# Optimization experiments

Hardware: AMD Instinct MI355X
Metric: run time of the kernel (lower is better)

The kernel has to match this reference:

```python
import jax, jax.numpy as jnp
import numpy as np

B, S, D, H = 2, 2048, 768, 12
DK = D // H


def setup_inputs() -> dict:
    key = jax.random.key(0)
    ks = jax.random.split(key, 10)
    sc = 0.02
    return {
        "k": jax.random.normal(ks[0], (B, S, D), jnp.float32),
        "q": jax.random.normal(ks[1], (B, S, D), jnp.float32),
        "v": jax.random.normal(ks[2], (B, S, D), jnp.float32),
        "mask": jnp.ones((B, 1, S, S), jnp.int32),
        "wq": jax.random.normal(ks[3], (D, D), jnp.float32) * sc,
        "bq": jnp.zeros((D,), jnp.float32),
        "wk": jax.random.normal(ks[4], (D, D), jnp.float32) * sc,
        "bk": jnp.zeros((D,), jnp.float32),
        "wv": jax.random.normal(ks[5], (D, D), jnp.float32) * sc,
        "bv": jnp.zeros((D,), jnp.float32),
        "wo": jax.random.normal(ks[6], (D, D), jnp.float32) * sc,
        "bo": jnp.zeros((D,), jnp.float32),
    }


def reference(k, q, v, mask, wq, bq, wk, bk, wv, bv, wo, bo):
    # Linear projections (torch Linear: x @ W^T + b)
    query = q @ wq.T + bq
    key_ = k @ wk.T + bk
    value = v @ wv.T + bv
    # [B,S,D] -> [B,H,S,DK]
    def split_heads(x):
        return x.reshape(B, S, H, DK).transpose(0, 2, 1, 3)
    Q, K, V = split_heads(query), split_heads(key_), split_heads(value)
    # NOTE: original masked_fill result is discarded -> mask is a no-op.
    scores = jnp.einsum("bhqd,bhkd->bhqk", Q, K) / jnp.sqrt(jnp.float32(DK))
    attn = jax.nn.softmax(scores, axis=-1)  # dropout p=0.0 -> identity
    out = jnp.einsum("bhqk,bhkd->bhqd", attn, V)
    out = out.transpose(0, 2, 1, 3).reshape(B, S, D)
    return out @ wo.T + bo
```

## Files before the change

### kernel.cpp

```cpp
#include <hip/hip_runtime.h>
#include <hip/hip_bf16.h>

#define B_  2
#define S_  2048
#define D_  768
#define H_  12
#define DK_ 64
#define NX_ (B_*S_*D_)
#define NW_ (D_*D_)
#define NR_ (B_*H_*S_)

typedef __attribute__((ext_vector_type(8))) short  bf16x8;
typedef __attribute__((ext_vector_type(4))) float  f32x4;

__device__ __forceinline__ unsigned short f2bf(float f) {
    unsigned int u = __float_as_uint(f);
    u += 0x7fffu + ((u >> 16) & 1u);
    return (unsigned short)(u >> 16);
}

__device__ __forceinline__ void async_cp16(const unsigned short* g,
                                           const unsigned short* lds_uniform_base) {
    __builtin_amdgcn_global_load_lds(
        (const __attribute__((address_space(1))) unsigned int*)(uintptr_t)g,
        (__attribute__((address_space(3))) unsigned int*)(unsigned int)(uintptr_t)lds_uniform_base,
        16, 0, 0);
}

__global__ __launch_bounds__(256) void cvt_w(const float* __restrict__ w0,
                                             const float* __restrict__ w1,
                                             const float* __restrict__ w2,
                                             const float* __restrict__ w3,
                                             unsigned short* __restrict__ dst) {
    const float* src[4] = {w0, w1, w2, w3};
    const int widx = blockIdx.y;
    const int idx  = blockIdx.x * 256 + threadIdx.x;
    const int n = idx / 96;
    const int g = idx % 96;
    const float4 f0 = *(const float4*)(src[widx] + (long)n * D_ + g * 8);
    const float4 f1 = *(const float4*)(src[widx] + (long)n * D_ + g * 8 + 4);
    unsigned short o[8] = {f2bf(f0.x), f2bf(f0.y), f2bf(f0.z), f2bf(f0.w),
                           f2bf(f1.x), f2bf(f1.y), f2bf(f1.z), f2bf(f1.w)};
    const int kdst = (g >> 3) * 64 + (((g & 7) ^ (n & 7)) * 8);
    *(uint4*)(dst + (long)widx * NW_ + (long)n * D_ + kdst) = *(const uint4*)o;
}

struct QkvArgs {
    const float* X[3];
    const float* bias[3];
    unsigned short* out[3];
};

__global__ __launch_bounds__(256, 2) void gemm_qkv(QkvArgs args,
                                                   const unsigned short* __restrict__ Wsw) {
    __shared__ __align__(16) unsigned short smem[17408];
    unsigned short* As = smem;
    unsigned short* Bs = smem + 8192;

    const int t    = threadIdx.x;
    const int wave = t >> 6;
    const int lane = t & 63;
    const int l16  = lane & 15;
    const int quad = lane >> 4;
    const int wm   = wave >> 1, wn = wave & 1;
    const int m0   = blockIdx.x * 128;
    const int zz   = blockIdx.y / 6;
    const int nb   = blockIdx.y % 6;
    const int n0   = nb * 128;

    const float* Xp = args.X[zz];
    const unsigned short* Wp = Wsw + (long)zz * NW_;

    f32x4 acc[4][4];
#pragma unroll
    for (int s = 0; s < 4; s++)
#pragma unroll
        for (int j = 0; j < 4; j++) acc[s][j] = (f32x4){0.f, 0.f, 0.f, 0.f};

    const int arow = t >> 3;
    const int acg  = t & 7;
    const int brow = lane >> 3;
    const int bcg  = lane & 7;

    for (int k0 = 0; k0 < D_; k0 += 64) {
        __syncthreads();
#pragma unroll
        for (int i = 0; i < 4; i++) {
            const int chunk = wave * 4 + i;
            async_cp16(Wp + (long)(n0 + chunk * 8 + brow) * D_ + k0 + bcg * 8,
                       Bs + chunk * 512);
        }
#pragma unroll
        for (int p = 0; p < 4; p++) {
            const int r = p * 32 + arow;
            const float4 f0 = *(const float4*)(Xp + (long)(m0 + r) * D_ + k0 + acg * 8);
            const float4 f1 = *(const float4*)(Xp + (long)(m0 + r) * D_ + k0 + acg * 8 + 4);
            unsigned short o[8] = {f2bf(f0.x), f2bf(f0.y), f2bf(f0.z), f2bf(f0.w),
                                   f2bf(f1.x), f2bf(f1.y), f2bf(f1.z), f2bf(f1.w)};
            *(uint4*)(As + r * 64 + ((acg ^ (r & 7)) * 8)) = *(const uint4*)o;
        }
        __syncthreads();
#pragma unroll
        for (int ks = 0; ks < 2; ks++) {
            const int cg = ks * 4 + quad;
            bf16x8 af[4], bf[4];
#pragma unroll
            for (int s = 0; s < 4; s++) {
                const int r = wm * 64 + s * 16 + l16;
                af[s] = *(const bf16x8*)&As[r * 64 + ((cg ^ (r & 7)) * 8)];
            }
#pragma unroll
            for (int j = 0; j < 4; j++) {
                const int r = wn * 64 + j * 16 + l16;
                bf[j] = *(const bf16x8*)&Bs[r * 64 + ((cg ^ (r & 7)) * 8)];
            }
#pragma unroll
            for (int s = 0; s < 4; s++)
#pragma unroll
                for (int j = 0; j < 4; j++)
                    acc[s][j] = __builtin_amdgcn_mfma_f32_16x16x32_bf16(af[s], bf[j], acc[s][j], 0, 0, 0);
        }
    }
    __syncthreads();

    const int b     = m0 >> 11;
    const int sbase = m0 & (S_ - 1);
    float bv[4];
#pragma unroll
    for (int j = 0; j < 4; j++) bv[j] = args.bias[zz][n0 + wn * 64 + j * 16 + l16];

    if (zz < 2) {
        unsigned short* Ls = smem;
#pragma unroll
        for (int s = 0; s < 4; s++)
#pragma unroll
            for (int j = 0; j < 4; j++)
#pragma unroll
                for (int r = 0; r < 4; r++)
                    Ls[(wm * 64 + s * 16 + quad * 4 + r) * 136 + wn * 64 + j * 16 + l16] =
                        f2bf(acc[s][j][r] + bv[j]);
        __syncthreads();
        const int row  = t >> 1;
        const int half = t & 1;
        unsigned short* Op = args.out[zz];
#pragma unroll
        for (int i = 0; i < 8; i++) {
            const int col  = half * 64 + i * 8;
            const int head = nb * 2 + half;
            const uint4 v = *(const uint4*)&Ls[row * 136 + col];
            *(uint4*)(Op + ((long)(b * H_ + head) * S_ + sbase + row) * DK_ + (col & 63)) = v;
        }
    } else {
        unsigned short* Ls = smem;
#pragma unroll
        for (int s = 0; s < 4; s++)
#pragma unroll
            for (int j = 0; j < 4; j++)
#pragma unroll
                for (int r = 0; r < 4; r++) {
                    const int dk  = j * 16 + l16;
                    const int pos = wm * 64 + (quad * 4 + r) * 4 + s;
                    Ls[wn * 8704 + dk * 136 + pos] = f2bf(acc[s][j][r] + bv[j]);
                }
        __syncthreads();
        const int rowIdx = t >> 1;
        const int hh = rowIdx >> 6, dk = rowIdx & 63;
        const int half = t & 1;
        unsigned short* Op = args.out[2];
#pragma unroll
        for (int i = 0; i < 8; i++) {
            const int col = half * 64 + i * 8;
            const uint4 v = *(const uint4*)&Ls[hh * 8704 + dk * 136 + col];
            const int head = nb * 2 + hh;
            *(uint4*)(Op + ((long)(b * H_ + head) * DK_ + dk) * S_ + sbase + col) = v;
        }
    }
}

__global__ __launch_bounds__(256, 3) void attn_kernel(
    const unsigned short* __restrict__ Q, const unsigned short* __restrict__ K,
    const unsigned short* __restrict__ Vt,
    float* __restrict__ Opart, float* __restrict__ Lp,
    unsigned short* __restrict__ Ao, int kvlen, int direct)
{
    const int t    = threadIdx.x;
    const int wave = t >> 6;
    const int lane = t & 63;
    const int l16  = lane & 15;
    const int quad = lane >> 4;
    const int qtile = blockIdx.x;
    const int bh    = blockIdx.y;
    const int z     = blockIdx.z;
    const int kvbase = z * kvlen;
    const int NIT    = kvlen >> 6;

    const unsigned short* Qp = Q  + (long)bh * S_ * DK_;
    const unsigned short* Kp = K  + (long)bh * S_ * DK_;
    const unsigned short* Vp = Vt + (long)bh * DK_ * S_;

    __shared__ __align__(16) unsigned short smem[18432];
    unsigned short* Ks = smem;
    unsigned short* Vs = smem + 4608;
    unsigned short* Ps = smem + 9216;

    bf16x8 qfrag[2][2];
#pragma unroll
    for (int st = 0; st < 2; st++) {
        const long qoff = (long)(qtile * 128 + wave * 32 + st * 16 + l16) * DK_ + quad * 8;
        qfrag[st][0] = *(const bf16x8*)(Qp + qoff);
        qfrag[st][1] = *(const bf16x8*)(Qp + qoff + 32);
    }

    const int srow = t >> 2;
    const int scg  = (t & 3) * 16;
    uint4 kreg[2], vreg[2];
    {
        const unsigned short* gk = Kp + (long)(kvbase + srow) * DK_ + scg;
        const unsigned short* gv = Vp + (long)srow * S_ + kvbase + scg;
        kreg[0] = *(const uint4*)gk;  kreg[1] = *(const uint4*)(gk + 8);
        vreg[0] = *(const uint4*)gv;  vreg[1] = *(const uint4*)(gv + 8);
    }

    f32x4 oacc[2][4];
#pragma unroll
    for (int st = 0; st < 2; st++)
#pragma unroll
        for (int j = 0; j < 4; j++) oacc[st][j] = (f32x4){0.f, 0.f, 0.f, 0.f};
    float lsum[2][4] = {{0.f,0.f,0.f,0.f},{0.f,0.f,0.f,0.f}};

    const float C = 0.18033688011112042f;

    for (int it = 0; it < NIT; ++it) {
        __syncthreads();
        *(uint4*)&Ks[srow * 72 + scg]     = kreg[0];
        *(uint4*)&Ks[srow * 72 + scg + 8] = kreg[1];
        *(uint4*)&Vs[srow * 72 + scg]     = vreg[0];
        *(uint4*)&Vs[srow * 72 + scg + 8] = vreg[1];
        __syncthreads();
        if (it + 1 < NIT) {
            const int kv0 = kvbase + (it + 1) * 64;
            const unsigned short* gk = Kp + (long)(kv0 + srow) * DK_ + scg;
            const unsigned short* gv = Vp + (long)srow * S_ + kv0 + scg;
            kreg[0] = *(const uint4*)gk;  kreg[1] = *(const uint4*)(gk + 8);
            vreg[0] = *(const uint4*)gv;  vreg[1] = *(const uint4*)(gv + 8);
        }

        f32x4 sacc[2][4];
#pragma unroll
        for (int st = 0; st < 2; st++)
#pragma unroll
            for (int j = 0; j < 4; j++) sacc[st][j] = (f32x4){0.f, 0.f, 0.f, 0.f};
#pragma unroll
        for (int ks = 0; ks < 2; ks++)
#pragma unroll
            for (int j = 0; j < 4; j++) {
                const bf16x8 bf = *(const bf16x8*)&Ks[(j * 16 + l16) * 72 + ks * 32 + quad * 8];
#pragma unroll
                for (int st = 0; st < 2; st++)
                    sacc[st][j] = __builtin_amdgcn_mfma_f32_16x16x32_bf16(qfrag[st][ks], bf, sacc[st][j], 0, 0, 0);
            }

#pragma unroll
        for (int st = 0; st < 2; st++)
#pragma unroll
            for (int r = 0; r < 4; r++) {
                unsigned short p4[4];
#pragma unroll
                for (int j = 0; j < 4; j++) {
                    const float p = exp2f(sacc[st][j][r] * C);
                    lsum[st][r] += p;
                    p4[j] = f2bf(p);
                }
                const int row = wave * 32 + st * 16 + quad * 4 + r;
                *(uint2*)&Ps[row * 72 + l16 * 4] = *(const uint2*)p4;
            }

#pragma unroll
        for (int st = 0; st < 2; st++)
#pragma unroll
            for (int ks = 0; ks < 2; ks++) {
                const bf16x8 pf = *(const bf16x8*)&Ps[(wave * 32 + st * 16 + l16) * 72 + ks * 32 + quad * 8];
#pragma unroll
                for (int j = 0; j < 4; j++) {
                    const bf16x8 vf = *(const bf16x8*)&Vs[(j * 16 + l16) * 72 + ks * 32 + quad * 8];
                    oacc[st][j] = __builtin_amdgcn_mfma_f32_16x16x32_bf16(pf, vf, oacc[st][j], 0, 0, 0);
                }
            }
    }

#pragma unroll
    for (int st = 0; st < 2; st++)
#pragma unroll
        for (int r = 0; r < 4; r++)
#pragma unroll
            for (int off = 1; off < 16; off <<= 1)
                lsum[st][r] += __shfl_xor(lsum[st][r], off, 64);

    if (direct) {
        const int b = bh / H_, h = bh % H_;
#pragma unroll
        for (int st = 0; st < 2; st++)
#pragma unroll
            for (int r = 0; r < 4; r++) {
                const float inv = 1.f / lsum[st][r];
                const int qrow = qtile * 128 + wave * 32 + st * 16 + quad * 4 + r;
#pragma unroll
                for (int j = 0; j < 4; j++)
                    Ao[(long)(b * S_ + qrow) * D_ + h * DK_ + j * 16 + l16] =
                        f2bf(oacc[st][j][r] * inv);
            }
    } else {
        float* Op = Opart + (long)z * NX_ + (long)bh * S_ * DK_;
        float* Lq = Lp + (long)z * NR_ + (long)bh * S_;
#pragma unroll
        for (int st = 0; st < 2; st++)
#pragma unroll
            for (int r = 0; r < 4; r++) {
                const int qrow = qtile * 128 + wave * 32 + st * 16 + quad * 4 + r;
#pragma unroll
                for (int j = 0; j < 4; j++)
                    Op[(long)qrow * DK_ + j * 16 + l16] = oacc[st][j][r];
                if (l16 == 0) Lq[qrow] = lsum[st][r];
            }
    }
}

__global__ __launch_bounds__(256) void combine_kernel(
    const float* __restrict__ Opart, const float* __restrict__ Lp,
    unsigned short* __restrict__ Ao)
{
    const long i = ((long)blockIdx.x * 256 + threadIdx.x) * 8;
    const int row = (int)(i >> 6);
    const float l = Lp[row] + Lp[NR_ + row];
    const float inv = 1.f / l;
    const float4 a0 = *(const float4*)(Opart + i);
    const float4 a1 = *(const float4*)(Opart + i + 4);
    const float4 b0 = *(const float4*)(Opart + NX_ + i);
    const float4 b1 = *(const float4*)(Opart + NX_ + i + 4);
    unsigned short o[8] = {
        f2bf((a0.x + b0.x) * inv), f2bf((a0.y + b0.y) * inv),
        f2bf((a0.z + b0.z) * inv), f2bf((a0.w + b0.w) * inv),
        f2bf((a1.x + b1.x) * inv), f2bf((a1.y + b1.y) * inv),
        f2bf((a1.z + b1.z) * inv), f2bf((a1.w + b1.w) * inv)};
    const int bh = row >> 11, s = row & (S_ - 1), dk0 = (int)(i & 63);
    const int b = bh / H_, h = bh % H_;
    *(uint4*)(Ao + (long)(b * S_ + s) * D_ + h * DK_ + dk0) = *(const uint4*)o;
}

__global__ __launch_bounds__(256, 2) void gemm_out(
    const unsigned short* __restrict__ A, const unsigned short* __restrict__ Wsw,
    const float* __restrict__ bias, float* __restrict__ Out)
{
    __shared__ __align__(16) unsigned short smem[8192];
    unsigned short* As = smem;
    unsigned short* Bs = smem + 4096;

    const int t    = threadIdx.x;
    const int wave = t >> 6;
    const int lane = t & 63;
    const int l16  = lane & 15;
    const int quad = lane >> 4;
    const int wm   = wave >> 1, wn = wave & 1;
    const int m0   = blockIdx.x * 64;
    const int n0   = blockIdx.y * 64;

    f32x4 acc[2][2];
#pragma unroll
    for (int s = 0; s < 2; s++)
#pragma unroll
        for (int j = 0; j < 2; j++) acc[s][j] = (f32x4){0.f, 0.f, 0.f, 0.f};

    const int arow = t >> 2;
    const int acg2 = (t & 3) * 2;
    const int brow = lane >> 3;
    const int bcg  = lane & 7;

    for (int k0 = 0; k0 < D_; k0 += 64) {
        __syncthreads();
#pragma unroll
        for (int i = 0; i < 2; i++) {
            const int chunk = wave * 2 + i;
            async_cp16(Wsw + (long)(n0 + chunk * 8 + brow) * D_ + k0 + bcg * 8,
                       Bs + chunk * 512);
        }
        {
            const uint4 v0 = *(const uint4*)(A + (long)(m0 + arow) * D_ + k0 + acg2 * 8);
            const uint4 v1 = *(const uint4*)(A + (long)(m0 + arow) * D_ + k0 + acg2 * 8 + 8);
            *(uint4*)(As + arow * 64 + ((acg2 ^ (arow & 7)) * 8))       = v0;
            *(uint4*)(As + arow * 64 + (((acg2 + 1) ^ (arow & 7)) * 8)) = v1;
        }
        __syncthreads();
#pragma unroll
        for (int ks = 0; ks < 2; ks++) {
            const int cg = ks * 4 + quad;
            bf16x8 af[2], bf[2];
#pragma unroll
            for (int s = 0; s < 2; s++) {
                const int r = wm * 32 + s * 16 + l16;
                af[s] = *(const bf16x8*)&As[r * 64 + ((cg ^ (r & 7)) * 8)];
            }
#pragma unroll
            for (int j = 0; j < 2; j++) {
                const int r = wn * 32 + j * 16 + l16;
                bf[j] = *(const bf16x8*)&Bs[r * 64 + ((cg ^ (r & 7)) * 8)];
            }
#pragma unroll
            for (int s = 0; s < 2; s++)
#pragma unroll
                for (int j = 0; j < 2; j++)
                    acc[s][j] = __builtin_amdgcn_mfma_f32_16x16x32_bf16(af[s], bf[j], acc[s][j], 0, 0, 0);
        }
    }

#pragma unroll
    for (int j = 0; j < 2; j++) {
        const int n = n0 + wn * 32 + j * 16 + l16;
        const float bv = bias[n];
#pragma unroll
        for (int s = 0; s < 2; s++)
#pragma unroll
            for (int r = 0; r < 4; r++) {
                const int m = m0 + wm * 32 + s * 16 + quad * 4 + r;
                Out[(long)m * D_ + n] = acc[s][j][r] + bv;
            }
    }
}

extern "C" void kernel_launch(void* const* d_in, const int* in_sizes, int n_in,
                              void* d_out, int out_size, void* d_ws, size_t ws_size,
                              hipStream_t stream) {
    const float* k_in = (const float*)d_in[0];
    const float* q_in = (const float*)d_in[1];
    const float* v_in = (const float*)d_in[2];
    const float* wq = (const float*)d_in[4];
    const float* bq = (const float*)d_in[5];
    const float* wk = (const float*)d_in[6];
    const float* bk = (const float*)d_in[7];
    const float* wv = (const float*)d_in[8];
    const float* bv = (const float*)d_in[9];
    const float* wo = (const float*)d_in[10];
    const float* bo = (const float*)d_in[11];

    unsigned short* ws = (unsigned short*)d_ws;
    unsigned short* Wsw = ws;
    unsigned short* Qb  = ws + 4ll * NW_;
    unsigned short* Kb  = Qb + (long)NX_;
    unsigned short* Vt  = Kb + (long)NX_;

    const size_t need_split = (4ull * NW_ + 3ull * NX_) * 2 + 2ull * NX_ * 4 + 2ull * NR_ * 4;
    const bool split = ws_size >= need_split;

    float* Opart = (float*)(Vt + (long)NX_);
    float* Lp    = Opart + 2ll * NX_;
    unsigned short* Ao = split ? Qb
                               : (unsigned short*)(Vt + (long)NX_);

    cvt_w<<<dim3(288, 4), 256, 0, stream>>>(wq, wk, wv, wo, Wsw);

    QkvArgs qa;
    qa.X[0] = q_in; qa.X[1] = k_in; qa.X[2] = v_in;
    qa.bias[0] = bq; qa.bias[1] = bk; qa.bias[2] = bv;
    qa.out[0] = Qb; qa.out[1] = Kb; qa.out[2] = Vt;
    gemm_qkv<<<dim3(32, 18), 256, 0, stream>>>(qa, Wsw);

    if (split) {
        attn_kernel<<<dim3(S_ / 128, B_ * H_, 2), 256, 0, stream>>>(
            Qb, Kb, Vt, Opart, Lp, nullptr, S_ / 2, 0);
        combine_kernel<<<dim3(NX_ / 2048), 256, 0, stream>>>(Opart, Lp, Ao);
    } else {
        attn_kernel<<<dim3(S_ / 128, B_ * H_, 1), 256, 0, stream>>>(
            Qb, Kb, Vt, nullptr, nullptr, Ao, S_, 1);
    }

    gemm_out<<<dim3(64, 12), 256, 0, stream>>>(Ao, Wsw + 3ll * NW_, bo, (float*)d_out);
}
```

Baseline: 241.4 us.

## Pre-convert inputs to swizzled bf16, fold softmax scale into Wq, retile output GEMM

Adds a cvt_x kernel that converts q/k/v activations to swizzled bf16 up front, so gemm_qkv can load A through async global-to-LDS copies instead of converting fp32 in the main loop. The softmax scale is folded into Wq and bq, which removes a multiply before each exp2 in attention. The P values are now packed with a cheaper perm-based bf16 conversion. Attention partial outputs and the gemm_out results are staged through LDS for coalesced float4 stores, and gemm_out moves to 128x128 tiles with the A operand stored pre-swizzled. The trade-off is an extra conversion pass over all three activations (a full bf16 round trip through memory) and a workspace region whose size is not reflected in the need_split check.

```diff
diff --git a/kernel.cpp b/kernel.cpp
--- a/kernel.cpp
+++ b/kernel.cpp
@@ -9,6 +9,7 @@
 #define NX_ (B_*S_*D_)
 #define NW_ (D_*D_)
 #define NR_ (B_*H_*S_)
+#define CSC 0.18033688011112042f
 
 typedef __attribute__((ext_vector_type(8))) short  bf16x8;
 typedef __attribute__((ext_vector_type(4))) float  f32x4;
@@ -17,6 +18,12 @@
     unsigned int u = __float_as_uint(f);
     u += 0x7fffu + ((u >> 16) & 1u);
     return (unsigned short)(u >> 16);
+}
+
+__device__ __forceinline__ unsigned pack_bf2(float a, float b) {
+    const unsigned ua = __float_as_uint(a) + 0x8000u;
+    const unsigned ub = __float_as_uint(b) + 0x8000u;
+    return __builtin_amdgcn_perm(ub, ua, 0x07060302u);
 }
 
 __device__ __forceinline__ void async_cp16(const unsigned short* g,
@@ -34,24 +41,39 @@
                                              unsigned short* __restrict__ dst) {
     const float* src[4] = {w0, w1, w2, w3};
     const int widx = blockIdx.y;
+    const float zs = (widx == 0) ? CSC : 1.0f;
     const int idx  = blockIdx.x * 256 + threadIdx.x;
     const int n = idx / 96;
     const int g = idx % 96;
     const float4 f0 = *(const float4*)(src[widx] + (long)n * D_ + g * 8);
     const float4 f1 = *(const float4*)(src[widx] + (long)n * D_ + g * 8 + 4);
+    unsigned short o[8] = {f2bf(f0.x*zs), f2bf(f0.y*zs), f2bf(f0.z*zs), f2bf(f0.w*zs),
+                           f2bf(f1.x*zs), f2bf(f1.y*zs), f2bf(f1.z*zs), f2bf(f1.w*zs)};
+    const int kdst = (g >> 3) * 64 + (((g & 7) ^ (n & 7)) * 8);
+    *(uint4*)(dst + (long)widx * NW_ + (long)n * D_ + kdst) = *(const uint4*)o;
+}
+
+__global__ __launch_bounds__(256) void cvt_x(const float* __restrict__ xq,
+                                             const float* __restrict__ xk,
+                                             const float* __restrict__ xv,
+                                             unsigned short* __restrict__ dst) {
+    const float* src[3] = {xq, xk, xv};
+    const int ten = blockIdx.y;
+    const int idx = blockIdx.x * 256 + threadIdx.x;
+    const int n = idx / 96;
+    const int g = idx % 96;
+    const float4 f0 = *(const float4*)(src[ten] + (long)n * D_ + g * 8);
+    const float4 f1 = *(const float4*)(src[ten] + (long)n * D_ + g * 8 + 4);
     unsigned short o[8] = {f2bf(f0.x), f2bf(f0.y), f2bf(f0.z), f2bf(f0.w),
                            f2bf(f1.x), f2bf(f1.y), f2bf(f1.z), f2bf(f1.w)};
     const int kdst = (g >> 3) * 64 + (((g & 7) ^ (n & 7)) * 8);
-    *(uint4*)(dst + (long)widx * NW_ + (long)n * D_ + kdst) = *(const uint4*)o;
-}
-
-struct QkvArgs {
-    const float* X[3];
-    const float* bias[3];
-    unsigned short* out[3];
-};
+    *(uint4*)(dst + (long)ten * NX_ + (long)n * D_ + kdst) = *(const uint4*)o;
+}
+
+struct QkvArgs { const float* bias[3]; unsigned short* out[3]; };
 
 __global__ __launch_bounds__(256, 2) void gemm_qkv(QkvArgs args,
+                                                   const unsigned short* __restrict__ Xsw,
                                                    const unsigned short* __restrict__ Wsw) {
     __shared__ __align__(16) unsigned short smem[17408];
     unsigned short* As = smem;
@@ -68,7 +90,7 @@
     const int nb   = blockIdx.y % 6;
     const int n0   = nb * 128;
 
-    const float* Xp = args.X[zz];
+    const unsigned short* Ap = Xsw + (long)zz * NX_;
     const unsigned short* Wp = Wsw + (long)zz * NW_;
 
     f32x4 acc[4][4];
@@ -77,27 +99,22 @@
 #pragma unroll
         for (int j = 0; j < 4; j++) acc[s][j] = (f32x4){0.f, 0.f, 0.f, 0.f};
 
-    const int arow = t >> 3;
-    const int acg  = t & 7;
-    const int brow = lane >> 3;
-    const int bcg  = lane & 7;
+    const int lrow = lane >> 3;
+    const int lcg  = lane & 7;
 
     for (int k0 = 0; k0 < D_; k0 += 64) {
         __syncthreads();
 #pragma unroll
         for (int i = 0; i < 4; i++) {
             const int chunk = wave * 4 + i;
-            async_cp16(Wp + (long)(n0 + chunk * 8 + brow) * D_ + k0 + bcg * 8,
+            async_cp16(Ap + (long)(m0 + chunk * 8 + lrow) * D_ + k0 + lcg * 8,
+                       As + chunk * 512);
+        }
+#pragma unroll
+        for (int i = 0; i < 4; i++) {
+            const int chunk = wave * 4 + i;
+            async_cp16(Wp + (long)(n0 + chunk * 8 + lrow) * D_ + k0 + lcg * 8,
                        Bs + chunk * 512);
-        }
-#pragma unroll
-        for (int p = 0; p < 4; p++) {
-            const int r = p * 32 + arow;
-            const float4 f0 = *(const float4*)(Xp + (long)(m0 + r) * D_ + k0 + acg * 8);
-            const float4 f1 = *(const float4*)(Xp + (long)(m0 + r) * D_ + k0 + acg * 8 + 4);
-            unsigned short o[8] = {f2bf(f0.x), f2bf(f0.y), f2bf(f0.z), f2bf(f0.w),
-                                   f2bf(f1.x), f2bf(f1.y), f2bf(f1.z), f2bf(f1.w)};
-            *(uint4*)(As + r * 64 + ((acg ^ (r & 7)) * 8)) = *(const uint4*)o;
         }
         __syncthreads();
 #pragma unroll
@@ -125,9 +142,10 @@
 
     const int b     = m0 >> 11;
     const int sbase = m0 & (S_ - 1);
+    const float zs  = (zz == 0) ? CSC : 1.0f;
     float bv[4];
 #pragma unroll
-    for (int j = 0; j < 4; j++) bv[j] = args.bias[zz][n0 + wn * 64 + j * 16 + l16];
+    for (int j = 0; j < 4; j++) bv[j] = args.bias[zz][n0 + wn * 64 + j * 16 + l16] * zs;
 
     if (zz < 2) {
         unsigned short* Ls = smem;
@@ -228,8 +246,6 @@
         for (int j = 0; j < 4; j++) oacc[st][j] = (f32x4){0.f, 0.f, 0.f, 0.f};
     float lsum[2][4] = {{0.f,0.f,0.f,0.f},{0.f,0.f,0.f,0.f}};
 
-    const float C = 0.18033688011112042f;
-
     for (int it = 0; it < NIT; ++it) {
         __syncthreads();
         *(uint4*)&Ks[srow * 72 + scg]     = kreg[0];
@@ -264,15 +280,14 @@
         for (int st = 0; st < 2; st++)
 #pragma unroll
             for (int r = 0; r < 4; r++) {
-                unsigned short p4[4];
-#pragma unroll
-                for (int j = 0; j < 4; j++) {
-                    const float p = exp2f(sacc[st][j][r] * C);
-                    lsum[st][r] += p;
-                    p4[j] = f2bf(p);
-                }
+                float p0 = exp2f(sacc[st][0][r]);
+                float p1 = exp2f(sacc[st][1][r]);
+                float p2 = exp2f(sacc[st][2][r]);
+                float p3 = exp2f(sacc[st][3][r]);
+                lsum[st][r] += (p0 + p1) + (p2 + p3);
+                uint2 pk = {pack_bf2(p0, p1), pack_bf2(p2, p3)};
                 const int row = wave * 32 + st * 16 + quad * 4 + r;
-                *(uint2*)&Ps[row * 72 + l16 * 4] = *(const uint2*)p4;
+                *(uint2*)&Ps[row * 72 + l16 * 4] = pk;
             }
 
 #pragma unroll
@@ -305,23 +320,39 @@
                 const float inv = 1.f / lsum[st][r];
                 const int qrow = qtile * 128 + wave * 32 + st * 16 + quad * 4 + r;
 #pragma unroll
-                for (int j = 0; j < 4; j++)
-                    Ao[(long)(b * S_ + qrow) * D_ + h * DK_ + j * 16 + l16] =
+                for (int j = 0; j < 4; j++) {
+                    const int dk = j * 16 + l16;
+                    const int dkw = ((dk >> 3) ^ (qrow & 7)) * 8 + (dk & 7);
+                    Ao[(long)(b * S_ + qrow) * D_ + h * DK_ + dkw] =
                         f2bf(oacc[st][j][r] * inv);
+                }
             }
     } else {
-        float* Op = Opart + (long)z * NX_ + (long)bh * S_ * DK_;
-        float* Lq = Lp + (long)z * NR_ + (long)bh * S_;
+        float* Lq = Lp + (long)z * NR_ + (long)bh * S_ + qtile * 128;
 #pragma unroll
         for (int st = 0; st < 2; st++)
 #pragma unroll
             for (int r = 0; r < 4; r++) {
-                const int qrow = qtile * 128 + wave * 32 + st * 16 + quad * 4 + r;
-#pragma unroll
-                for (int j = 0; j < 4; j++)
-                    Op[(long)qrow * DK_ + j * 16 + l16] = oacc[st][j][r];
-                if (l16 == 0) Lq[qrow] = lsum[st][r];
-            }
+                const int row = wave * 32 + st * 16 + quad * 4 + r;
+                if (l16 == 0) Lq[row] = lsum[st][r];
+            }
+        __syncthreads();
+        float* fl = (float*)smem;
+#pragma unroll
+        for (int st = 0; st < 2; st++)
+#pragma unroll
+            for (int j = 0; j < 4; j++)
+#pragma unroll
+                for (int r = 0; r < 4; r++)
+                    fl[(wave * 32 + st * 16 + quad * 4 + r) * 67 + j * 16 + l16] = oacc[st][j][r];
+        __syncthreads();
+        float* Op = Opart + (long)z * NX_ + (long)bh * S_ * DK_ + (long)qtile * 128 * DK_;
+        const int row = t >> 1, c0 = (t & 1) * 32;
+#pragma unroll
+        for (int i = 0; i < 8; i++) {
+            const float4 v = *(const float4*)&fl[row * 67 + c0 + i * 4];
+            *(float4*)(Op + row * DK_ + c0 + i * 4) = v;
+        }
     }
 }
 
@@ -331,8 +362,7 @@
 {
     const long i = ((long)blockIdx.x * 256 + threadIdx.x) * 8;
     const int row = (int)(i >> 6);
-    const float l = Lp[row] + Lp[NR_ + row];
-    const float inv = 1.f / l;
+    const float inv = 1.f / (Lp[row] + Lp[NR_ + row]);
     const float4 a0 = *(const float4*)(Opart + i);
     const float4 a1 = *(const float4*)(Opart + i + 4);
     const float4 b0 = *(const float4*)(Opart + NX_ + i);
@@ -342,18 +372,20 @@
         f2bf((a0.z + b0.z) * inv), f2bf((a0.w + b0.w) * inv),
         f2bf((a1.x + b1.x) * inv), f2bf((a1.y + b1.y) * inv),
         f2bf((a1.z + b1.z) * inv), f2bf((a1.w + b1.w) * inv)};
-    const int bh = row >> 11, s = row & (S_ - 1), dk0 = (int)(i & 63);
+    const int bh = row >> 11, s = row & (S_ - 1);
     const int b = bh / H_, h = bh % H_;
-    *(uint4*)(Ao + (long)(b * S_ + s) * D_ + h * DK_ + dk0) = *(const uint4*)o;
+    const int g8 = (int)(i & 63) >> 3;
+    const int dkw = ((g8 ^ (s & 7)) * 8);
+    *(uint4*)(Ao + (long)(b * S_ + s) * D_ + h * DK_ + dkw) = *(const uint4*)o;
 }
 
 __global__ __launch_bounds__(256, 2) void gemm_out(
     const unsigned short* __restrict__ A, const unsigned short* __restrict__ Wsw,
     const float* __restrict__ bias, float* __restrict__ Out)
 {
-    __shared__ __align__(16) unsigned short smem[8192];
+    __shared__ __align__(16) unsigned short smem[17408];
     unsigned short* As = smem;
-    unsigned short* Bs = smem + 4096;
+    unsigned short* Bs = smem + 8192;
 
     const int t    = threadIdx.x;
     const int wave = t >> 6;
@@ -361,68 +393,80 @@
     const int l16  = lane & 15;
     const int quad = lane >> 4;
     const int wm   = wave >> 1, wn = wave & 1;
-    const int m0   = blockIdx.x * 64;
-    const int n0   = blockIdx.y * 64;
-
-    f32x4 acc[2][2];
-#pragma unroll
-    for (int s = 0; s < 2; s++)
-#pragma unroll
-        for (int j = 0; j < 2; j++) acc[s][j] = (f32x4){0.f, 0.f, 0.f, 0.f};
-
-    const int arow = t >> 2;
-    const int acg2 = (t & 3) * 2;
-    const int brow = lane >> 3;
-    const int bcg  = lane & 7;
+    const int m0   = blockIdx.x * 128;
+    const int n0   = blockIdx.y * 128;
+
+    f32x4 acc[4][4];
+#pragma unroll
+    for (int s = 0; s < 4; s++)
+#pragma unroll
+        for (int j = 0; j < 4; j++) acc[s][j] = (f32x4){0.f, 0.f, 0.f, 0.f};
+
+    const int lrow = lane >> 3;
+    const int lcg  = lane & 7;
 
     for (int k0 = 0; k0 < D_; k0 += 64) {
         __syncthreads();
 #pragma unroll
-        for (int i = 0; i < 2; i++) {
-            const int chunk = wave * 2 + i;
-            async_cp16(Wsw + (long)(n0 + chunk * 8 + brow) * D_ + k0 + bcg * 8,
+        for (int i = 0; i < 4; i++) {
+            const int chunk = wave * 4 + i;
+            async_cp16(A + (long)(m0 + chunk * 8 + lrow) * D_ + k0 + lcg * 8,
+                       As + chunk * 512);
+        }
+#pragma unroll
+        for (int i = 0; i < 4; i++) {
+            const int chunk = wave * 4 + i;
+            async_cp16(Wsw + (long)(n0 + chunk * 8 + lrow) * D_ + k0 + lcg * 8,
                        Bs + chunk * 512);
-        }
-        {
-            const uint4 v0 = *(const uint4*)(A + (long)(m0 + arow) * D_ + k0 + acg2 * 8);
-            const uint4 v1 = *(const uint4*)(A + (long)(m0 + arow) * D_ + k0 + acg2 * 8 + 8);
-            *(uint4*)(As + arow * 64 + ((acg2 ^ (arow & 7)) * 8))       = v0;
-            *(uint4*)(As + arow * 64 + (((acg2 + 1) ^ (arow & 7)) * 8)) = v1;
         }
         __syncthreads();
 #pragma unroll
         for (int ks = 0; ks < 2; ks++) {
             const int cg = ks * 4 + quad;
-            bf16x8 af[2], bf[2];
-#pragma unroll
-            for (int s = 0; s < 2; s++) {
-                const int r = wm * 32 + s * 16 + l16;
+            bf16x8 af[4], bf[4];
+#pragma unroll
+            for (int s = 0; s < 4; s++) {
+                const int r = wm * 64 + s * 16 + l16;
                 af[s] = *(const bf16x8*)&As[r * 64 + ((cg ^ (r & 7)) * 8)];
             }
 #pragma unroll
-            for (int j = 0; j < 2; j++) {
-                const int r = wn * 32 + j * 16 + l16;
+            for (int j = 0; j < 4; j++) {
+                const int r = wn * 64 + j * 16 + l16;
                 bf[j] = *(const bf16x8*)&Bs[r * 64 + ((cg ^ (r & 7)) * 8)];
             }
 #pragma unroll
-            for (int s = 0; s < 2; s++)
-#pragma unroll
-                for (int j = 0; j < 2; j++)
+            for (int s = 0; s < 4; s++)
+#pragma unroll
+                for (int j = 0; j < 4; j++)
                     acc[s][j] = __builtin_amdgcn_mfma_f32_16x16x32_bf16(af[s], bf[j], acc[s][j], 0, 0, 0);
         }
     }
 
-#pragma unroll
-    for (int j = 0; j < 2; j++) {
-        const int n = n0 + wn * 32 + j * 16 + l16;
-        const float bv = bias[n];
-#pragma unroll
-        for (int s = 0; s < 2; s++)
-#pragma unroll
-            for (int r = 0; r < 4; r++) {
-                const int m = m0 + wm * 32 + s * 16 + quad * 4 + r;
-                Out[(long)m * D_ + n] = acc[s][j][r] + bv;
-            }
+    float bv[4];
+#pragma unroll
+    for (int j = 0; j < 4; j++) bv[j] = bias[n0 + wn * 64 + j * 16 + l16];
+
+    float* fl = (float*)smem;
+#pragma unroll
+    for (int h = 0; h < 2; h++) {
+        __syncthreads();
+        if (wn == h) {
+#pragma unroll
+            for (int s = 0; s < 4; s++)
+#pragma unroll
+                for (int j = 0; j < 4; j++)
+#pragma unroll
+                    for (int r = 0; r < 4; r++)
+                        fl[(wm * 64 + s * 16 + quad * 4 + r) * 67 + j * 16 + l16] =
+                            acc[s][j][r] + bv[j];
+        }
+        __syncthreads();
+        const int row = t >> 1, c0 = (t & 1) * 32;
+#pragma unroll
+        for (int i = 0; i < 8; i++) {
+            const float4 v = *(const float4*)&fl[row * 67 + c0 + i * 4];
+            *(float4*)(Out + (long)(m0 + row) * D_ + n0 + h * 64 + c0 + i * 4) = v;
+        }
     }
 }
 
@@ -443,34 +487,35 @@
 
     unsigned short* ws = (unsigned short*)d_ws;
     unsigned short* Wsw = ws;
-    unsigned short* Qb  = ws + 4ll * NW_;
+    unsigned short* Qb  = Wsw + 4ll * NW_;
     unsigned short* Kb  = Qb + (long)NX_;
     unsigned short* Vt  = Kb + (long)NX_;
-
-    const size_t need_split = (4ull * NW_ + 3ull * NX_) * 2 + 2ull * NX_ * 4 + 2ull * NR_ * 4;
+    unsigned short* Xsw = Vt + (long)NX_;
+
+    const size_t need_split = (4ull*NW_ + 3ull*NX_)*2 + 2ull*NX_*4 + 2ull*NR_*4;
     const bool split = ws_size >= need_split;
 
-    float* Opart = (float*)(Vt + (long)NX_);
+    float* Opart = (float*)Xsw;
     float* Lp    = Opart + 2ll * NX_;
     unsigned short* Ao = split ? Qb
-                               : (unsigned short*)(Vt + (long)NX_);
+                               : Xsw;
 
     cvt_w<<<dim3(288, 4), 256, 0, stream>>>(wq, wk, wv, wo, Wsw);
+    cvt_x<<<dim3(1536, 3), 256, 0, stream>>>(q_in, k_in, v_in, Xsw);
 
     QkvArgs qa;
-    qa.X[0] = q_in; qa.X[1] = k_in; qa.X[2] = v_in;
     qa.bias[0] = bq; qa.bias[1] = bk; qa.bias[2] = bv;
-    qa.out[0] = Qb; qa.out[1] = Kb; qa.out[2] = Vt;
-    gemm_qkv<<<dim3(32, 18), 256, 0, stream>>>(qa, Wsw);
+    qa.out[0] = Qb;  qa.out[1] = Kb;  qa.out[2] = Vt;
+    gemm_qkv<<<dim3(32, 18), 256, 0, stream>>>(qa, Xsw, Wsw);
 
     if (split) {
-        attn_kernel<<<dim3(S_ / 128, B_ * H_, 2), 256, 0, stream>>>(
-            Qb, Kb, Vt, Opart, Lp, nullptr, S_ / 2, 0);
-        combine_kernel<<<dim3(NX_ / 2048), 256, 0, stream>>>(Opart, Lp, Ao);
+        attn_kernel<<<dim3(S_/128, B_*H_, 2), 256, 0, stream>>>(
+            Qb, Kb, Vt, Opart, Lp, nullptr, S_/2, 0);
+        combine_kernel<<<dim3(NX_/2048), 256, 0, stream>>>(Opart, Lp, Ao);
     } else {
-        attn_kernel<<<dim3(S_ / 128, B_ * H_, 1), 256, 0, stream>>>(
+        attn_kernel<<<dim3(S_/128, B_*H_, 1), 256, 0, stream>>>(
             Qb, Kb, Vt, nullptr, nullptr, Ao, S_, 1);
     }
 
-    gemm_out<<<dim3(64, 12), 256, 0, stream>>>(Ao, Wsw + 3ll * NW_, bo, (float*)d_out);
-}
+    gemm_out<<<dim3(32, 6), 256, 0, stream>>>(Ao, Wsw + 3ll*NW_, bo, (float*)d_out);
+}
```

After: 250.6 us. +3.8%, slower.
